# Optimization experiments

Measured on AMD Instinct MI355X. Metric: run time of the kernel, lower is better.

## Reference

```python
import jax, jax.numpy as jnp
import numpy as np

NH, DK, DV = 8, 10, 10  # num_heads, per-head key dim, per-head value dim (dim_k=dim_v=80)


def setup_inputs() -> dict:
    key = jax.random.key(0)
    k1, k2, k3, k4, k5 = jax.random.split(key, 5)
    B, NX, NY = 64, 512, 512
    x = jax.random.normal(k1, (B, NX, 768), dtype=jnp.float32)
    y = jax.random.normal(k2, (B, NY, 283), dtype=jnp.float32)
    # nn.Linear(bias=False) weights, stored transposed as (in, out); scaled init
    Wq = jax.random.normal(k3, (768, 80), dtype=jnp.float32) * 0.02
    Wk = jax.random.normal(k4, (283, 80), dtype=jnp.float32) * 0.02
    Wv = jax.random.normal(k5, (283, 80), dtype=jnp.float32) * 0.02
    return {"x": x, "y": y, "Wq": Wq, "Wk": Wk, "Wv": Wv}


def reference(x, y, Wq, Wk, Wv):
    B, nx, _ = x.shape
    ny = y.shape[1]
    # projections -> split heads: (B, nh, seq, dhead)
    q = (x @ Wq).reshape(B, nx, NH, DK).transpose(0, 2, 1, 3)
    k = (y @ Wk).reshape(B, ny, NH, DK).transpose(0, 2, 1, 3)
    v = (y @ Wv).reshape(B, ny, NH, DV).transpose(0, 2, 1, 3)
    scale = 1.0 / np.sqrt(DK).astype(np.float32)
    dist = jax.nn.softmax(jnp.einsum("bhqd,bhkd->bhqk", q, k) * scale, axis=-1)
    att = q + jnp.einsum("bhqk,bhkd->bhqd", dist, v)  # residual add of q
    att = att.transpose(0, 2, 1, 3).reshape(B, nx, NH * DV)
    # module returns `result` = flattened attention (fc/BN stack is dead code)
    return att.reshape(B, -1)
```

## Files before the change

### kernel.cpp

```cpp
#include <hip/hip_runtime.h>
#include <stdint.h>

typedef unsigned short u16;
typedef unsigned int   u32;
typedef _Float16       f16;

typedef __attribute__((ext_vector_type(2))) _Float16 half2v;
typedef __attribute__((ext_vector_type(4))) _Float16 half4v;
typedef __attribute__((ext_vector_type(8))) _Float16 half8v;
typedef __attribute__((ext_vector_type(4))) float    floatx4;

#define NXS    512
#define NYS    512
#define NHEAD  8
#define DHEAD  10
#define DMODEL 80
#define DXK    768
#define DYK    283
#define DYKP   288

__device__ inline half2v pk2(float x, float y) {
  return __builtin_bit_cast(half2v, __builtin_amdgcn_cvt_pkrtz(x, y));
}
__device__ inline half4v cvt4(float4 v) {
  return __builtin_shufflevector(pk2(v.x, v.y), pk2(v.z, v.w), 0, 1, 2, 3);
}
__device__ inline half4v h4u32(u32 a, u32 b) {
  return __builtin_shufflevector(__builtin_bit_cast(half2v, a),
                                 __builtin_bit_cast(half2v, b), 0, 1, 2, 3);
}

__global__ __launch_bounds__(256) void w_prep(const float* __restrict__ Wq,
                                              const float* __restrict__ Wk,
                                              const float* __restrict__ Wv,
                                              f16* __restrict__ Tq,
                                              f16* __restrict__ Tk,
                                              f16* __restrict__ Tv) {
  const int idx = blockIdx.x * 256 + threadIdx.x;
  if (idx < 80 * 768) {
    const int c = idx / 768, k = idx - c * 768;
    Tq[idx] = (f16)Wq[k * 80 + c];
  }
  if (idx < 80 * 288) {
    const int c = idx / 288, k = idx - c * 288;
    float a = 0.f, b = 0.f;
    if (k < DYK) { a = Wk[k * 80 + c]; b = Wv[k * 80 + c]; }
    Tk[idx] = (f16)a;
    Tv[idx] = (f16)b;
  }
}

__global__ __launch_bounds__(256) void proj(const float* __restrict__ X,
                                            const float* __restrict__ Y,
                                            const f16* __restrict__ Wtq,
                                            const f16* __restrict__ Wtk,
                                            const f16* __restrict__ Wtv,
                                            f16* __restrict__ Qw,
                                            f16* __restrict__ Kw,
                                            f16* __restrict__ Vw) {
  const int t = threadIdx.x;
  const int wv = t >> 6, lane = t & 63, m16 = lane & 15, quad = lane >> 4;
  const int blk = blockIdx.x;

  if (blk < 512) {
    __shared__ f16 Xs[64 * 40];
    __shared__ f16 Ws[80 * 40];
    const int row0 = blk * 64;
    const int xr_r = t >> 3, xr_k = (t & 7) << 2;
    const int wi0 = t, wi1 = t + 160;

    float4 xr0, xr1;
    uint4 wr0, wr1;
    xr0 = *(const float4*)&X[(size_t)(row0 + xr_r) * DXK + xr_k];
    xr1 = *(const float4*)&X[(size_t)(row0 + xr_r + 32) * DXK + xr_k];
    if (t < 160) {
      wr0 = *(const uint4*)&Wtq[(wi0 >> 2) * DXK + (wi0 & 3) * 8];
      wr1 = *(const uint4*)&Wtq[(wi1 >> 2) * DXK + (wi1 & 3) * 8];
    }

    floatx4 acc[5];
#pragma unroll
    for (int i = 0; i < 5; ++i) acc[i] = (floatx4){0.f, 0.f, 0.f, 0.f};

    for (int s = 0; s < 24; ++s) {
      if (s) __syncthreads();
      *(half4v*)&Xs[xr_r * 40 + xr_k] = cvt4(xr0);
      *(half4v*)&Xs[(xr_r + 32) * 40 + xr_k] = cvt4(xr1);
      if (t < 160) {
        *(uint4*)&Ws[(wi0 >> 2) * 40 + (wi0 & 3) * 8] = wr0;
        *(uint4*)&Ws[(wi1 >> 2) * 40 + (wi1 & 3) * 8] = wr1;
      }
      __syncthreads();
      if (s < 23) {
        const int k0 = (s + 1) * 32;
        xr0 = *(const float4*)&X[(size_t)(row0 + xr_r) * DXK + k0 + xr_k];
        xr1 = *(const float4*)&X[(size_t)(row0 + xr_r + 32) * DXK + k0 + xr_k];
        if (t < 160) {
          wr0 = *(const uint4*)&Wtq[(wi0 >> 2) * DXK + k0 + (wi0 & 3) * 8];
          wr1 = *(const uint4*)&Wtq[(wi1 >> 2) * DXK + k0 + (wi1 & 3) * 8];
        }
      }
      const half8v a = *(const half8v*)&Xs[(wv * 16 + m16) * 40 + quad * 8];
#pragma unroll
      for (int nt = 0; nt < 5; ++nt) {
        const half8v b = *(const half8v*)&Ws[(nt * 16 + m16) * 40 + quad * 8];
        acc[nt] = __builtin_amdgcn_mfma_f32_16x16x32_f16(a, b, acc[nt], 0, 0, 0);
      }
    }
#pragma unroll
    for (int nt = 0; nt < 5; ++nt) {
      const int col = nt * 16 + m16;
#pragma unroll
      for (int p = 0; p < 4; ++p) {
        const int grow = row0 + wv * 16 + quad * 4 + p;
        Qw[(size_t)grow * DMODEL + col] = (f16)acc[nt][p];
      }
    }
  } else {
    __shared__ f16 Ys[64 * 40];
    __shared__ f16 Wks[80 * 40];
    __shared__ f16 Wvs[80 * 40];
    const int row0 = (blk - 512) * 64;
    const int wi0 = t, wi1 = t + 160;

    float yr[8];
    uint4 wk0, wk1, wv0, wv1;
#pragma unroll
    for (int i = 0; i < 8; ++i) {
      const int idx = t + 256 * i;
      const int r = idx >> 5, kk = idx & 31;
      yr[i] = Y[(size_t)(row0 + r) * DYK + kk];
    }
    if (t < 160) {
      wk0 = *(const uint4*)&Wtk[(wi0 >> 2) * DYKP + (wi0 & 3) * 8];
      wk1 = *(const uint4*)&Wtk[(wi1 >> 2) * DYKP + (wi1 & 3) * 8];
      wv0 = *(const uint4*)&Wtv[(wi0 >> 2) * DYKP + (wi0 & 3) * 8];
      wv1 = *(const uint4*)&Wtv[(wi1 >> 2) * DYKP + (wi1 & 3) * 8];
    }

    floatx4 ak[5], av[5];
#pragma unroll
    for (int i = 0; i < 5; ++i) {
      ak[i] = (floatx4){0.f, 0.f, 0.f, 0.f};
      av[i] = (floatx4){0.f, 0.f, 0.f, 0.f};
    }

    for (int s = 0; s < 9; ++s) {
      if (s) __syncthreads();
#pragma unroll
      for (int i = 0; i < 8; ++i) {
        const int idx = t + 256 * i;
        Ys[(idx >> 5) * 40 + (idx & 31)] = (f16)yr[i];
      }
      if (t < 160) {
        *(uint4*)&Wks[(wi0 >> 2) * 40 + (wi0 & 3) * 8] = wk0;
        *(uint4*)&Wks[(wi1 >> 2) * 40 + (wi1 & 3) * 8] = wk1;
        *(uint4*)&Wvs[(wi0 >> 2) * 40 + (wi0 & 3) * 8] = wv0;
        *(uint4*)&Wvs[(wi1 >> 2) * 40 + (wi1 & 3) * 8] = wv1;
      }
      __syncthreads();
      if (s < 8) {
        const int k0 = (s + 1) * 32;
#pragma unroll
        for (int i = 0; i < 8; ++i) {
          const int idx = t + 256 * i;
          const int r = idx >> 5, k = k0 + (idx & 31);
          yr[i] = (k < DYK) ? Y[(size_t)(row0 + r) * DYK + k] : 0.f;
        }
        if (t < 160) {
          wk0 = *(const uint4*)&Wtk[(wi0 >> 2) * DYKP + k0 + (wi0 & 3) * 8];
          wk1 = *(const uint4*)&Wtk[(wi1 >> 2) * DYKP + k0 + (wi1 & 3) * 8];
          wv0 = *(const uint4*)&Wtv[(wi0 >> 2) * DYKP + k0 + (wi0 & 3) * 8];
          wv1 = *(const uint4*)&Wtv[(wi1 >> 2) * DYKP + k0 + (wi1 & 3) * 8];
        }
      }
      const half8v a = *(const half8v*)&Ys[(wv * 16 + m16) * 40 + quad * 8];
#pragma unroll
      for (int nt = 0; nt < 5; ++nt) {
        const half8v bk = *(const half8v*)&Wks[(nt * 16 + m16) * 40 + quad * 8];
        ak[nt] = __builtin_amdgcn_mfma_f32_16x16x32_f16(a, bk, ak[nt], 0, 0, 0);
        const half8v bv = *(const half8v*)&Wvs[(nt * 16 + m16) * 40 + quad * 8];
        av[nt] = __builtin_amdgcn_mfma_f32_16x16x32_f16(a, bv, av[nt], 0, 0, 0);
      }
    }
#pragma unroll
    for (int nt = 0; nt < 5; ++nt) {
      const int col = nt * 16 + m16;
      const int h = col / 10, d = col - h * 10;
#pragma unroll
      for (int p = 0; p < 4; ++p) {
        const int grow = row0 + wv * 16 + quad * 4 + p;
        const int bb = grow >> 9, ny = grow & 511;
        const size_t o = (((size_t)bb * NHEAD + h) * NYS + ny) * DHEAD + d;
        Kw[o] = (f16)ak[nt][p];
        Vw[o] = (f16)av[nt][p];
      }
    }
  }
}

__global__ __launch_bounds__(256) void attn(const f16* __restrict__ Q,
                                            const f16* __restrict__ K,
                                            const f16* __restrict__ V,
                                            float* __restrict__ O) {
  __shared__ f16 Ks[512 * 22];
  __shared__ f16 Vt[16 * 522];
  const int t = threadIdx.x;
  const int wv = t >> 6, lane = t & 63, m16 = lane & 15, quad = lane >> 4;
  const int bh = blockIdx.x >> 1, half = blockIdx.x & 1;
  const int b = bh >> 3, h = bh & 7;

  const u32* Kg = (const u32*)K + (size_t)bh * NYS * 5;
  const u32* Vg = (const u32*)V + (size_t)bh * NYS * 5;
  for (int idx = t; idx < 2560; idx += 256) {
    const u32 row = (u32)idx / 5u, c = (u32)idx - row * 5u;
    const half2v kv = __builtin_bit_cast(half2v, Kg[idx]);
    Ks[row * 22 + 2 * c]     = kv[0];
    Ks[row * 22 + 2 * c + 1] = kv[1];
    const half2v vvv = __builtin_bit_cast(half2v, Vg[idx]);
    Vt[(2 * c) * 522 + row]     = vvv[0];
    Vt[(2 * c + 1) * 522 + row] = vvv[1];
  }
  for (int idx = t; idx < 3072; idx += 256) {
    const u32 row = (u32)idx / 6u, d = 10u + ((u32)idx - row * 6u);
    Ks[row * 22 + d] = (f16)0.f;
  }
  for (int idx = t; idx < 6 * 522; idx += 256)
    Vt[10 * 522 + idx] = (f16)0.f;
  __syncthreads();

  const float scale = 0.31622776601683794f;
#pragma unroll 1
  for (int i = 0; i < 4; ++i) {
    const int qt = half * 16 + wv * 4 + i;
    const int qrow = qt * 16 + m16;
    const u32* Qg32 = (const u32*)(Q + ((size_t)b * NXS + qrow) * DMODEL + h * DHEAD);
    float s0 = 0.f, s1 = 0.f, s2 = 0.f, s3 = 0.f;
    if (quad < 2) {
      const u32 ua = Qg32[quad * 2], ub = Qg32[quad * 2 + 1];
      const half2v ha = __builtin_bit_cast(half2v, ua);
      const half2v hb = __builtin_bit_cast(half2v, ub);
      s0 = (float)ha[0]; s1 = (float)ha[1]; s2 = (float)hb[0]; s3 = (float)hb[1];
    } else if (quad == 2) {
      const u32 ua = Qg32[4];
      const half2v ha = __builtin_bit_cast(half2v, ua);
      s0 = (float)ha[0]; s1 = (float)ha[1];
    }
    const half4v qf = __builtin_shufflevector(pk2(s0 * scale, s1 * scale),
                                              pk2(s2 * scale, s3 * scale),
                                              0, 1, 2, 3);
    floatx4 o0 = (floatx4){0.f, 0.f, 0.f, 0.f};
    floatx4 o1 = (floatx4){0.f, 0.f, 0.f, 0.f};
    float l0 = 0.f, l1 = 0.f;
    for (int kt = 0; kt < 32; kt += 2) {
#pragma unroll
      for (int u = 0; u < 2; ++u) {
        const int ktu = kt + u;
        const int kb = (ktu * 16 + m16) * 22 + quad * 4;
        const half4v kf = h4u32(*(const u32*)&Ks[kb], *(const u32*)&Ks[kb + 2]);
        const floatx4 s = __builtin_amdgcn_mfma_f32_16x16x16f16(
            kf, qf, (floatx4){0.f, 0.f, 0.f, 0.f}, 0, 0, 0);
        const float p0 = __expf(s[0]);
        const float p1 = __expf(s[1]);
        const float p2 = __expf(s[2]);
        const float p3 = __expf(s[3]);
        const half4v pf = __builtin_shufflevector(pk2(p0, p1), pk2(p2, p3),
                                                  0, 1, 2, 3);
        const int vb = m16 * 522 + ktu * 16 + quad * 4;
        const half4v vf = h4u32(*(const u32*)&Vt[vb], *(const u32*)&Vt[vb + 2]);
        if (u == 0) {
          l0 += (p0 + p1) + (p2 + p3);
          o0 = __builtin_amdgcn_mfma_f32_16x16x16f16(pf, vf, o0, 0, 0, 0);
        } else {
          l1 += (p0 + p1) + (p2 + p3);
          o1 = __builtin_amdgcn_mfma_f32_16x16x16f16(pf, vf, o1, 0, 0, 0);
        }
      }
    }
    float lp = l0 + l1;
    lp += __shfl_xor(lp, 16);
    lp += __shfl_xor(lp, 32);
#pragma unroll
    for (int p = 0; p < 4; ++p) {
      const int rq = qt * 16 + quad * 4 + p;
      const float lr = __shfl(lp, quad * 4 + p);
      if (m16 < DHEAD) {
        const float qres = (float)Q[((size_t)b * NXS + rq) * DMODEL + h * DHEAD + m16];
        O[((size_t)b * NXS + rq) * DMODEL + h * DHEAD + m16] =
            qres + (o0[p] + o1[p]) / lr;
      }
    }
  }
}

extern "C" void kernel_launch(void* const* d_in, const int* in_sizes, int n_in,
                              void* d_out, int out_size, void* d_ws, size_t ws_size,
                              hipStream_t stream) {
  const float* x  = (const float*)d_in[0];
  const float* y  = (const float*)d_in[1];
  const float* Wq = (const float*)d_in[2];
  const float* Wk = (const float*)d_in[3];
  const float* Wv = (const float*)d_in[4];
  float* out = (float*)d_out;

  char* ws = (char*)d_ws;
  f16* Wtq = (f16*)(ws);
  f16* Wtk = (f16*)(ws + 122880);
  f16* Wtv = (f16*)(ws + 168960);
  f16* Qw  = (f16*)(ws + 262144);
  f16* Kw  = (f16*)(ws + 5505024);
  f16* Vw  = (f16*)(ws + 10747904);

  w_prep<<<240, 256, 0, stream>>>(Wq, Wk, Wv, Wtq, Wtk, Wtv);
  proj  <<<1024, 256, 0, stream>>>(x, y, Wtq, Wtk, Wtv, Qw, Kw, Vw);
  attn  <<<1024, 256, 0, stream>>>(Qw, Kw, Vw, out);
}
```

Baseline: 237.0 us.

## Deepen projection prefetch pipeline, share LDS, and store K/V row-major

The Q projection now keeps three k-slices of X and W in flight in registers, and the K/V projection keeps two, instead of one, so more global-load latency can hide behind MFMA work. Both branches of the projection kernel now carve their tiles from one shared char buffer, so LDS use per block is the larger branch rather than the sum of both. K and V are written in row-major (B, ny, 80) layout instead of head-split, which gives contiguous stores, and the attention kernel reads its head slice with a strided index. Costs are higher register pressure (possibly lower occupancy) and less coalesced 4-byte gathers in the attention load.

Measured after the change: 285.9 us. 20.6% more time.

```diff
diff --git a/kernel.cpp b/kernel.cpp
--- a/kernel.cpp
+++ b/kernel.cpp
@@ -58,46 +58,53 @@
                                             f16* __restrict__ Qw,
                                             f16* __restrict__ Kw,
                                             f16* __restrict__ Vw) {
+  __shared__ __align__(16) char smem[17920];
   const int t = threadIdx.x;
   const int wv = t >> 6, lane = t & 63, m16 = lane & 15, quad = lane >> 4;
   const int blk = blockIdx.x;
 
   if (blk < 512) {
-    __shared__ f16 Xs[64 * 40];
-    __shared__ f16 Ws[80 * 40];
+    f16* Xs = (f16*)smem;
+    f16* Ws = (f16*)(smem + 5120);
     const int row0 = blk * 64;
     const int xr_r = t >> 3, xr_k = (t & 7) << 2;
     const int wi0 = t, wi1 = t + 160;
 
-    float4 xr0, xr1;
-    uint4 wr0, wr1;
-    xr0 = *(const float4*)&X[(size_t)(row0 + xr_r) * DXK + xr_k];
-    xr1 = *(const float4*)&X[(size_t)(row0 + xr_r + 32) * DXK + xr_k];
-    if (t < 160) {
-      wr0 = *(const uint4*)&Wtq[(wi0 >> 2) * DXK + (wi0 & 3) * 8];
-      wr1 = *(const uint4*)&Wtq[(wi1 >> 2) * DXK + (wi1 & 3) * 8];
+    float4 xa[3], xb[3];
+    uint4 wr0[3], wr1[3];
+#pragma unroll
+    for (int j = 0; j < 3; ++j) {
+      const int k0 = j * 32;
+      xa[j] = *(const float4*)&X[(size_t)(row0 + xr_r) * DXK + k0 + xr_k];
+      xb[j] = *(const float4*)&X[(size_t)(row0 + xr_r + 32) * DXK + k0 + xr_k];
+      if (t < 160) {
+        wr0[j] = *(const uint4*)&Wtq[(wi0 >> 2) * DXK + k0 + (wi0 & 3) * 8];
+        wr1[j] = *(const uint4*)&Wtq[(wi1 >> 2) * DXK + k0 + (wi1 & 3) * 8];
+      }
     }
 
     floatx4 acc[5];
 #pragma unroll
     for (int i = 0; i < 5; ++i) acc[i] = (floatx4){0.f, 0.f, 0.f, 0.f};
 
+#pragma unroll 3
     for (int s = 0; s < 24; ++s) {
+      const int j = s % 3;
       if (s) __syncthreads();
-      *(half4v*)&Xs[xr_r * 40 + xr_k] = cvt4(xr0);
-      *(half4v*)&Xs[(xr_r + 32) * 40 + xr_k] = cvt4(xr1);
+      *(half4v*)&Xs[xr_r * 40 + xr_k] = cvt4(xa[j]);
+      *(half4v*)&Xs[(xr_r + 32) * 40 + xr_k] = cvt4(xb[j]);
       if (t < 160) {
-        *(uint4*)&Ws[(wi0 >> 2) * 40 + (wi0 & 3) * 8] = wr0;
-        *(uint4*)&Ws[(wi1 >> 2) * 40 + (wi1 & 3) * 8] = wr1;
+        *(uint4*)&Ws[(wi0 >> 2) * 40 + (wi0 & 3) * 8] = wr0[j];
+        *(uint4*)&Ws[(wi1 >> 2) * 40 + (wi1 & 3) * 8] = wr1[j];
       }
       __syncthreads();
-      if (s < 23) {
-        const int k0 = (s + 1) * 32;
-        xr0 = *(const float4*)&X[(size_t)(row0 + xr_r) * DXK + k0 + xr_k];
-        xr1 = *(const float4*)&X[(size_t)(row0 + xr_r + 32) * DXK + k0 + xr_k];
+      if (s + 3 < 24) {
+        const int k0 = (s + 3) * 32;
+        xa[j] = *(const float4*)&X[(size_t)(row0 + xr_r) * DXK + k0 + xr_k];
+        xb[j] = *(const float4*)&X[(size_t)(row0 + xr_r + 32) * DXK + k0 + xr_k];
         if (t < 160) {
-          wr0 = *(const uint4*)&Wtq[(wi0 >> 2) * DXK + k0 + (wi0 & 3) * 8];
-          wr1 = *(const uint4*)&Wtq[(wi1 >> 2) * DXK + k0 + (wi1 & 3) * 8];
+          wr0[j] = *(const uint4*)&Wtq[(wi0 >> 2) * DXK + k0 + (wi0 & 3) * 8];
+          wr1[j] = *(const uint4*)&Wtq[(wi1 >> 2) * DXK + k0 + (wi1 & 3) * 8];
         }
       }
       const half8v a = *(const half8v*)&Xs[(wv * 16 + m16) * 40 + quad * 8];
@@ -117,25 +124,29 @@
       }
     }
   } else {
-    __shared__ f16 Ys[64 * 40];
-    __shared__ f16 Wks[80 * 40];
-    __shared__ f16 Wvs[80 * 40];
+    f16* Ys  = (f16*)smem;
+    f16* Wks = (f16*)(smem + 5120);
+    f16* Wvs = (f16*)(smem + 11520);
     const int row0 = (blk - 512) * 64;
     const int wi0 = t, wi1 = t + 160;
 
-    float yr[8];
-    uint4 wk0, wk1, wv0, wv1;
-#pragma unroll
-    for (int i = 0; i < 8; ++i) {
-      const int idx = t + 256 * i;
-      const int r = idx >> 5, kk = idx & 31;
-      yr[i] = Y[(size_t)(row0 + r) * DYK + kk];
-    }
-    if (t < 160) {
-      wk0 = *(const uint4*)&Wtk[(wi0 >> 2) * DYKP + (wi0 & 3) * 8];
-      wk1 = *(const uint4*)&Wtk[(wi1 >> 2) * DYKP + (wi1 & 3) * 8];
-      wv0 = *(const uint4*)&Wtv[(wi0 >> 2) * DYKP + (wi0 & 3) * 8];
-      wv1 = *(const uint4*)&Wtv[(wi1 >> 2) * DYKP + (wi1 & 3) * 8];
+    float yr[2][8];
+    uint4 wk0[2], wk1[2], wv0[2], wv1[2];
+#pragma unroll
+    for (int j = 0; j < 2; ++j) {
+      const int k0 = j * 32;
+#pragma unroll
+      for (int i = 0; i < 8; ++i) {
+        const int idx = t + 256 * i;
+        const int r = idx >> 5, kk = idx & 31;
+        yr[j][i] = Y[(size_t)(row0 + r) * DYK + k0 + kk];
+      }
+      if (t < 160) {
+        wk0[j] = *(const uint4*)&Wtk[(wi0 >> 2) * DYKP + k0 + (wi0 & 3) * 8];
+        wk1[j] = *(const uint4*)&Wtk[(wi1 >> 2) * DYKP + k0 + (wi1 & 3) * 8];
+        wv0[j] = *(const uint4*)&Wtv[(wi0 >> 2) * DYKP + k0 + (wi0 & 3) * 8];
+        wv1[j] = *(const uint4*)&Wtv[(wi1 >> 2) * DYKP + k0 + (wi1 & 3) * 8];
+      }
     }
 
     floatx4 ak[5], av[5];
@@ -145,33 +156,43 @@
       av[i] = (floatx4){0.f, 0.f, 0.f, 0.f};
     }
 
+#pragma unroll 2
     for (int s = 0; s < 9; ++s) {
+      const int j = s & 1;
       if (s) __syncthreads();
 #pragma unroll
       for (int i = 0; i < 8; ++i) {
         const int idx = t + 256 * i;
-        Ys[(idx >> 5) * 40 + (idx & 31)] = (f16)yr[i];
+        Ys[(idx >> 5) * 40 + (idx & 31)] = (f16)yr[j][i];
       }
       if (t < 160) {
-        *(uint4*)&Wks[(wi0 >> 2) * 40 + (wi0 & 3) * 8] = wk0;
-        *(uint4*)&Wks[(wi1 >> 2) * 40 + (wi1 & 3) * 8] = wk1;
-        *(uint4*)&Wvs[(wi0 >> 2) * 40 + (wi0 & 3) * 8] = wv0;
-        *(uint4*)&Wvs[(wi1 >> 2) * 40 + (wi1 & 3) * 8] = wv1;
+        *(uint4*)&Wks[(wi0 >> 2) * 40 + (wi0 & 3) * 8] = wk0[j];
+        *(uint4*)&Wks[(wi1 >> 2) * 40 + (wi1 & 3) * 8] = wk1[j];
+        *(uint4*)&Wvs[(wi0 >> 2) * 40 + (wi0 & 3) * 8] = wv0[j];
+        *(uint4*)&Wvs[(wi1 >> 2) * 40 + (wi1 & 3) * 8] = wv1[j];
       }
       __syncthreads();
-      if (s < 8) {
-        const int k0 = (s + 1) * 32;
-#pragma unroll
-        for (int i = 0; i < 8; ++i) {
-          const int idx = t + 256 * i;
-          const int r = idx >> 5, k = k0 + (idx & 31);
-          yr[i] = (k < DYK) ? Y[(size_t)(row0 + r) * DYK + k] : 0.f;
+      if (s + 2 < 9) {
+        const int k0 = (s + 2) * 32;
+        if (s + 2 < 8) {
+#pragma unroll
+          for (int i = 0; i < 8; ++i) {
+            const int idx = t + 256 * i;
+            yr[j][i] = Y[(size_t)(row0 + (idx >> 5)) * DYK + k0 + (idx & 31)];
+          }
+        } else {
+#pragma unroll
+          for (int i = 0; i < 8; ++i) {
+            const int idx = t + 256 * i;
+            const int k = k0 + (idx & 31);
+            yr[j][i] = (k < DYK) ? Y[(size_t)(row0 + (idx >> 5)) * DYK + k] : 0.f;
+          }
         }
         if (t < 160) {
-          wk0 = *(const uint4*)&Wtk[(wi0 >> 2) * DYKP + k0 + (wi0 & 3) * 8];
-          wk1 = *(const uint4*)&Wtk[(wi1 >> 2) * DYKP + k0 + (wi1 & 3) * 8];
-          wv0 = *(const uint4*)&Wtv[(wi0 >> 2) * DYKP + k0 + (wi0 & 3) * 8];
-          wv1 = *(const uint4*)&Wtv[(wi1 >> 2) * DYKP + k0 + (wi1 & 3) * 8];
+          wk0[j] = *(const uint4*)&Wtk[(wi0 >> 2) * DYKP + k0 + (wi0 & 3) * 8];
+          wk1[j] = *(const uint4*)&Wtk[(wi1 >> 2) * DYKP + k0 + (wi1 & 3) * 8];
+          wv0[j] = *(const uint4*)&Wtv[(wi0 >> 2) * DYKP + k0 + (wi0 & 3) * 8];
+          wv1[j] = *(const uint4*)&Wtv[(wi1 >> 2) * DYKP + k0 + (wi1 & 3) * 8];
         }
       }
       const half8v a = *(const half8v*)&Ys[(wv * 16 + m16) * 40 + quad * 8];
@@ -186,14 +207,11 @@
 #pragma unroll
     for (int nt = 0; nt < 5; ++nt) {
       const int col = nt * 16 + m16;
-      const int h = col / 10, d = col - h * 10;
 #pragma unroll
       for (int p = 0; p < 4; ++p) {
         const int grow = row0 + wv * 16 + quad * 4 + p;
-        const int bb = grow >> 9, ny = grow & 511;
-        const size_t o = (((size_t)bb * NHEAD + h) * NYS + ny) * DHEAD + d;
-        Kw[o] = (f16)ak[nt][p];
-        Vw[o] = (f16)av[nt][p];
+        Kw[(size_t)grow * DMODEL + col] = (f16)ak[nt][p];
+        Vw[(size_t)grow * DMODEL + col] = (f16)av[nt][p];
       }
     }
   }
@@ -210,14 +228,14 @@
   const int bh = blockIdx.x >> 1, half = blockIdx.x & 1;
   const int b = bh >> 3, h = bh & 7;
 
-  const u32* Kg = (const u32*)K + (size_t)bh * NYS * 5;
-  const u32* Vg = (const u32*)V + (size_t)bh * NYS * 5;
+  const u32* Kg = (const u32*)K + (size_t)b * NXS * 40 + h * 5;
+  const u32* Vg = (const u32*)V + (size_t)b * NXS * 40 + h * 5;
   for (int idx = t; idx < 2560; idx += 256) {
     const u32 row = (u32)idx / 5u, c = (u32)idx - row * 5u;
-    const half2v kv = __builtin_bit_cast(half2v, Kg[idx]);
+    const half2v kv = __builtin_bit_cast(half2v, Kg[row * 40 + c]);
     Ks[row * 22 + 2 * c]     = kv[0];
     Ks[row * 22 + 2 * c + 1] = kv[1];
-    const half2v vvv = __builtin_bit_cast(half2v, Vg[idx]);
+    const half2v vvv = __builtin_bit_cast(half2v, Vg[row * 40 + c]);
     Vt[(2 * c) * 522 + row]     = vvv[0];
     Vt[(2 * c + 1) * 522 + row] = vvv[1];
   }
```
